# Performance work log

Hardware: AMD Instinct MI355X
Metric: run time of the kernel (lower is better)

## Reference

```python
import jax, jax.numpy as jnp
import numpy as np

GAMMA = 1.0  # get_gamma(1, None) == 1


def setup_inputs() -> dict:
    key = jax.random.key(0)
    # scale down so recursion divisors 1 - km^2 stay well-conditioned
    a = jax.random.normal(key, (2048, 1024, 33), dtype=jnp.float32) * 0.05
    return {"a": a}


def reference(a):
    # LPC -> PARCOR (reverse Levinson-Durbin recursion), a: [..., M+1]
    M = a.shape[-1] - 1
    K = a[..., :1]          # gain term, passed through
    ar = a[..., 1:] * GAMMA  # working LPC coefficients, length M
    ks = []
    # Python loop over the (small, fixed) LPC order; fully vectorized over batch.
    for m in range(M - 1, -1, -1):
        km = ar[..., m:m + 1]           # reflection coefficient k_m
        ks.append(km)
        if m == 0:
            break
        z = 1.0 - km * km
        k = ar[..., :m]                 # step-down: shrink order by one
        ar = (k - km * k[..., ::-1]) / z
    ks.append(K)
    return jnp.concatenate(ks[::-1], axis=-1)
```

## Files before the change

### kernel.cpp

```cpp
#include <hip/hip_runtime.h>

#define M 32
#define NC 33
#define TPB 64
#define ROWS 128
#define FPB (ROWS * NC)
#define V4R 16
#define TAILF 4096

typedef float f4 __attribute__((ext_vector_type(4)));
typedef float f2 __attribute__((ext_vector_type(2)));

__global__ __launch_bounds__(TPB, 2)
void lpc_to_parcor_kernel(const float* __restrict__ a,
                          float* __restrict__ out,
                          long long nrows) {
    __shared__ float lds[FPB];
    const int t = threadIdx.x;
    const long long base = (long long)blockIdx.x * FPB;
    const long long limit = nrows * NC;
    const bool full = (base + FPB) <= limit;

    if (full) {
        const f4* g4 = (const f4*)(a + base);
        f4* l4 = (f4*)lds;
#pragma unroll
        for (int k = 0; k < V4R; ++k)
            l4[t + k * TPB] = g4[t + k * TPB];
        lds[TAILF + t]       = a[base + TAILF + t];
        lds[TAILF + TPB + t] = a[base + TAILF + TPB + t];
    } else {
        for (int k = 0; k < 66; ++k) {
            int g = t + k * TPB;
            long long ga = base + g;
            lds[g] = (ga < limit) ? a[ga] : 0.0f;
        }
    }
    __syncthreads();

    const int rb0 = t * NC;
    const int rb1 = t * NC + 64 * NC;
    f2 ar[M];
#pragma unroll
    for (int j = 0; j < M; ++j) {
        ar[j].x = lds[rb0 + 1 + j];
        ar[j].y = lds[rb1 + 1 + j];
    }
#pragma unroll
    for (int m = M - 1; m >= 1; --m) {
        f2 km = ar[m];
        lds[rb0 + m + 1] = km.x;
        lds[rb1 + m + 1] = km.y;
        f2 z = 1.0f - km * km;
        f2 r;
        r.x = 1.0f / z.x;
        r.y = 1.0f / z.y;
        const int h = m >> 1;
#pragma unroll
        for (int j = 0; j < h; ++j) {
            f2 x = ar[j], y = ar[m - 1 - j];
            ar[j]         = (x - km * y) * r;
            ar[m - 1 - j] = (y - km * x) * r;
        }
        if (m & 1) ar[h] = (ar[h] - km * ar[h]) * r;
    }
    lds[rb0 + 1] = ar[0].x;
    lds[rb1 + 1] = ar[0].y;
    __syncthreads();

    if (full) {
        const f4* l4 = (const f4*)lds;
#pragma unroll
        for (int k = 0; k < V4R; ++k) {
            f4 v = l4[t + k * TPB];
            __builtin_nontemporal_store(v, (f4*)(out + base) + t + k * TPB);
        }
        __builtin_nontemporal_store(lds[TAILF + t],       out + base + TAILF + t);
        __builtin_nontemporal_store(lds[TAILF + TPB + t], out + base + TAILF + TPB + t);
    } else {
        for (int k = 0; k < 66; ++k) {
            int g = t + k * TPB;
            long long ga = base + g;
            if (ga < limit) out[ga] = lds[g];
        }
    }
}

extern "C" void kernel_launch(void* const* d_in, const int* in_sizes, int n_in,
                              void* d_out, int out_size, void* d_ws, size_t ws_size,
                              hipStream_t stream) {
    const float* a = (const float*)d_in[0];
    float* out = (float*)d_out;
    long long nrows = (long long)in_sizes[0] / NC;
    long long ntiles = (nrows + ROWS - 1) / ROWS;
    lpc_to_parcor_kernel<<<(int)ntiles, TPB, 0, stream>>>(a, out, nrows);
}
```

Before: 94.43 us.

## Use persistent blocks with double-buffered async global-to-LDS DMA prefetch

The kernel becomes persistent: 1024 blocks each loop over a contiguous range of tiles. Each block double-buffers LDS and issues global_load_lds DMA for the next tile while it runs the Levinson recursion and stores the current one. Tile loads now overlap with compute and stores instead of running one tile per block. In exchange, LDS per block doubles, occupancy drops to one block per CU, and the block relies on manual vmcnt waits with no barriers between DMA and LDS reads. Those waits may be wrong because the nontemporal stores are also counted in vmcnt.

```diff
diff --git a/kernel.cpp b/kernel.cpp
--- a/kernel.cpp
+++ b/kernel.cpp
@@ -7,37 +7,34 @@
 #define FPB (ROWS * NC)
 #define V4R 16
 #define TAILF 4096
+#define NBLOCKS 1024
+#define DMA_N 18
 
 typedef float f4 __attribute__((ext_vector_type(4)));
+
+__device__ __forceinline__ void dma16(const float* g, float* l) {
+    __builtin_amdgcn_global_load_lds(
+        (const __attribute__((address_space(1))) unsigned int*)g,
+        (__attribute__((address_space(3))) unsigned int*)l, 16, 0, 0);
+}
+__device__ __forceinline__ void dma4(const float* g, float* l) {
+    __builtin_amdgcn_global_load_lds(
+        (const __attribute__((address_space(1))) unsigned int*)g,
+        (__attribute__((address_space(3))) unsigned int*)l, 4, 0, 0);
+}
+
+__device__ __forceinline__ void issue_tile_dma(const float* __restrict__ src,
+                                               float* __restrict__ lbuf, int lane) {
+#pragma unroll
+    for (int k = 0; k < 16; ++k)
+        dma16(src + k * 256 + lane * 4, lbuf + k * 256);
+#pragma unroll
+    for (int r = 0; r < 2; ++r)
+        dma4(src + TAILF + r * 64 + lane, lbuf + TAILF + r * 64);
+}
+
 typedef float f2 __attribute__((ext_vector_type(2)));
-
-__global__ __launch_bounds__(TPB, 2)
-void lpc_to_parcor_kernel(const float* __restrict__ a,
-                          float* __restrict__ out,
-                          long long nrows) {
-    __shared__ float lds[FPB];
-    const int t = threadIdx.x;
-    const long long base = (long long)blockIdx.x * FPB;
-    const long long limit = nrows * NC;
-    const bool full = (base + FPB) <= limit;
-
-    if (full) {
-        const f4* g4 = (const f4*)(a + base);
-        f4* l4 = (f4*)lds;
-#pragma unroll
-        for (int k = 0; k < V4R; ++k)
-            l4[t + k * TPB] = g4[t + k * TPB];
-        lds[TAILF + t]       = a[base + TAILF + t];
-        lds[TAILF + TPB + t] = a[base + TAILF + TPB + t];
-    } else {
-        for (int k = 0; k < 66; ++k) {
-            int g = t + k * TPB;
-            long long ga = base + g;
-            lds[g] = (ga < limit) ? a[ga] : 0.0f;
-        }
-    }
-    __syncthreads();
-
+__device__ __forceinline__ void levinson2(float* __restrict__ lds, int t) {
     const int rb0 = t * NC;
     const int rb1 = t * NC + 64 * NC;
     f2 ar[M];
@@ -66,23 +63,76 @@
     }
     lds[rb0 + 1] = ar[0].x;
     lds[rb1 + 1] = ar[0].y;
+}
+
+__device__ __forceinline__ void store_tile_nt(float* __restrict__ dst,
+                                              const float* __restrict__ lds, int t) {
+    const f4* l4 = (const f4*)lds;
+#pragma unroll
+    for (int k = 0; k < V4R; ++k) {
+        f4 v = l4[t + k * TPB];
+        __builtin_nontemporal_store(v, (f4*)dst + t + k * TPB);
+    }
+    __builtin_nontemporal_store(lds[TAILF + t],       dst + TAILF + t);
+    __builtin_nontemporal_store(lds[TAILF + TPB + t], dst + TAILF + TPB + t);
+}
+
+__device__ __forceinline__ void process_tile_guarded(float* __restrict__ lds,
+                                                     const float* __restrict__ a,
+                                                     float* __restrict__ out,
+                                                     long long base, long long limit, int t) {
+    for (int k = 0; k < 66; ++k) {
+        int g = t + k * TPB;
+        long long ga = base + g;
+        lds[g] = (ga < limit) ? a[ga] : 0.0f;
+    }
     __syncthreads();
+    levinson2(lds, t);
+    __syncthreads();
+    for (int k = 0; k < 66; ++k) {
+        int g = t + k * TPB;
+        long long ga = base + g;
+        if (ga < limit) out[ga] = lds[g];
+    }
+    __syncthreads();
+}
 
-    if (full) {
-        const f4* l4 = (const f4*)lds;
-#pragma unroll
-        for (int k = 0; k < V4R; ++k) {
-            f4 v = l4[t + k * TPB];
-            __builtin_nontemporal_store(v, (f4*)(out + base) + t + k * TPB);
+__global__ __launch_bounds__(TPB, 1)
+void lpc_to_parcor_kernel(const float* __restrict__ a,
+                          float* __restrict__ out,
+                          long long nrows, long long tiles_per_block) {
+    __shared__ float lds[2 * FPB];
+    const int t = threadIdx.x;
+    const long long limit = nrows * NC;
+    const long long ntiles = (nrows + ROWS - 1) / ROWS;
+    const long long nfull  = nrows / ROWS;
+
+    long long t0 = (long long)blockIdx.x * tiles_per_block;
+    long long t1 = t0 + tiles_per_block; if (t1 > ntiles) t1 = ntiles;
+    if (t0 >= t1) return;
+    long long fend = (t1 < nfull) ? t1 : nfull;
+
+    if (t0 < fend) {
+        issue_tile_dma(a + t0 * FPB, lds, t);
+
+        for (long long ti = t0; ti < fend; ++ti) {
+            float* cur = lds + ((int)((ti - t0) & 1)) * FPB;
+            float* nxt = lds + ((int)((ti - t0 + 1) & 1)) * FPB;
+
+            if (ti == t0) asm volatile("s_waitcnt vmcnt(0)"  ::: "memory");
+            else          asm volatile("s_waitcnt vmcnt(18)" ::: "memory");
+
+            if (ti + 1 < fend) issue_tile_dma(a + (ti + 1) * FPB, nxt, t);
+
+            levinson2(cur, t);
+
+            store_tile_nt(out + ti * FPB, cur, t);
         }
-        __builtin_nontemporal_store(lds[TAILF + t],       out + base + TAILF + t);
-        __builtin_nontemporal_store(lds[TAILF + TPB + t], out + base + TAILF + TPB + t);
-    } else {
-        for (int k = 0; k < 66; ++k) {
-            int g = t + k * TPB;
-            long long ga = base + g;
-            if (ga < limit) out[ga] = lds[g];
-        }
+    }
+    for (long long ti = (t0 > nfull ? t0 : nfull); ti < t1; ++ti) {
+        asm volatile("s_waitcnt vmcnt(0)" ::: "memory");
+        __syncthreads();
+        process_tile_guarded(lds, a, out, ti * FPB, limit, t);
     }
 }
 
@@ -93,5 +143,7 @@
     float* out = (float*)d_out;
     long long nrows = (long long)in_sizes[0] / NC;
     long long ntiles = (nrows + ROWS - 1) / ROWS;
-    lpc_to_parcor_kernel<<<(int)ntiles, TPB, 0, stream>>>(a, out, nrows);
+    long long blocks = (ntiles < NBLOCKS) ? ntiles : NBLOCKS;
+    long long tpb_tiles = (ntiles + blocks - 1) / blocks;
+    lpc_to_parcor_kernel<<<(int)blocks, TPB, 0, stream>>>(a, out, nrows, tpb_tiles);
 }
```

After: 111.2 us. 1.18x slower.
